# Optimization experiments

Hardware: AMD Instinct MI355X
Metric: run time of the kernel (lower is better)

Reference implementation:

```python
import jax, jax.numpy as jnp
import numpy as np

N_NODES = 50000


def setup_inputs() -> dict:
    key = jax.random.key(0)
    k1, k2, k3, k4 = jax.random.split(key, 4)
    x = jax.random.normal(k1, (N_NODES, 256), dtype=jnp.float32)
    edge_index = jax.random.randint(k2, (2, 800000), 0, N_NODES, dtype=jnp.int64)
    W1 = jax.random.normal(k3, (256, 128), dtype=jnp.float32) * (1.0 / np.sqrt(256))
    b1 = jnp.zeros((128,), dtype=jnp.float32)
    W2 = jax.random.normal(k4, (128, 16), dtype=jnp.float32) * (1.0 / np.sqrt(128))
    b2 = jnp.zeros((16,), dtype=jnp.float32)
    return {"x": x, "edge_index": edge_index, "W1": W1, "b1": b1, "W2": W2, "b2": b2}


def _gcn_norm(edge_index, num_nodes):
    # add self-loops, then symmetric normalization D^-1/2 A D^-1/2 (PyG GCNConv default)
    loop = jnp.arange(num_nodes, dtype=edge_index.dtype)
    src = jnp.concatenate([edge_index[0], loop])
    dst = jnp.concatenate([edge_index[1], loop])
    deg = jax.ops.segment_sum(jnp.ones_like(dst, dtype=jnp.float32), dst, num_segments=num_nodes)
    dinv = jnp.where(deg > 0, jax.lax.rsqrt(deg), 0.0)
    norm = dinv[src] * dinv[dst]  # [E+N]
    return src, dst, norm


def _gcn_conv(h, W, b, src, dst, norm, num_nodes):
    h = h @ W                             # linear before propagate
    msg = h[src] * norm[:, None]          # gather + edge scaling
    agg = jax.ops.segment_sum(msg, dst, num_segments=num_nodes)  # scatter-add
    return agg + b


def reference(x, edge_index, W1, b1, W2, b2):
    n = x.shape[0]
    src, dst, norm = _gcn_norm(edge_index, n)
    h = jax.nn.relu(_gcn_conv(x, W1, b1, src, dst, norm, n))
    # F.dropout(training=False) is identity in eval mode
    out = _gcn_conv(h, W2, b2, src, dst, norm, n)
    return jax.nn.log_softmax(out, axis=1)
```

## Files before the change

kernel.cpp:

```cpp
#include <hip/hip_runtime.h>
#include <hip/hip_bf16.h>
#include <math.h>


#define FIN 256
#define FH  128
#define FO  16
#define ECH_LOG 13
#define ECH (1 << ECH_LOG)
#define NCHUNK 98
#define WPH 6272

typedef unsigned int uint;
typedef unsigned short ushort;
typedef __attribute__((ext_vector_type(8))) short bf16x8;
typedef __attribute__((ext_vector_type(4))) float f32x4;

static __device__ __forceinline__ ushort f2bf(float f) {
    __hip_bfloat16 b = __float2bfloat16(f);
    return *reinterpret_cast<ushort*>(&b);
}
static __device__ __forceinline__ float bf2f(ushort u) {
    return __uint_as_float(((uint)u) << 16);
}

__global__ __launch_bounds__(256) void GCN_wprep_k(const float* __restrict__ W1,
                                                   ushort* __restrict__ whT,
                                                   ushort* __restrict__ wlT) {
    int i = blockIdx.x * 256 + threadIdx.x;
    int k = i >> 7, c = i & 127;
    float w = W1[i];
    ushort hh = f2bf(w);
    ushort hl = f2bf(w - bf2f(hh));
    whT[c * 256 + k] = hh;
    wlT[c * 256 + k] = hl;
}

#define G1_BR 64
#define G1_KC 32

__global__ __launch_bounds__(256, 4) void GCN_histgemm_k(
        const float* __restrict__ x, const ushort* __restrict__ whT,
        const ushort* __restrict__ wlT, ushort* __restrict__ h1,
        const int* __restrict__ edge, uint* __restrict__ cw,
        int* __restrict__ rank,
        int N, int E, int nHist, int nWords, int wph) {
    __shared__ __align__(16) char smem[WPH * 4];
    int tid = threadIdx.x;

    if ((int)blockIdx.x < nHist) {
        int bid = blockIdx.x;
        int half = bid & 1;
        int c = bid >> 1;
        uint* lh = (uint*)smem;
        int w0 = half * wph;
        int wlim = nWords - w0; if (wlim > wph) wlim = wph;
        for (int j = tid; j < wlim; j += 256) lh[j] = 0;
        __syncthreads();
        int base = c << ECH_LOG;
        int lim = base + ECH; if (lim > E) lim = E;
        for (int i = base + tid; i < lim; i += 256) {
            int d = edge[E + i];
            int wd = (d >> 2) - w0;
            if ((unsigned)wd < (unsigned)wlim) {
                int sh = (d & 3) << 3;
                uint old = atomicAdd(&lh[wd], 1u << sh);
                rank[i] = (int)((old >> sh) & 0xFFu);
            }
        }
        __syncthreads();
        for (int j = tid; j < wlim; j += 256)
            cw[(size_t)c * nWords + w0 + j] = lh[j];
        return;
    }

    ushort* xh_s = (ushort*)smem;
    ushort* xl_s = (ushort*)(smem + 4096);
    ushort* wh_s = (ushort*)(smem + 8192);
    ushort* wl_s = (ushort*)(smem + 16384);
    int row0 = (blockIdx.x - nHist) * G1_BR;
    int ln = tid & 63;
    int w  = tid >> 6;
    int ln15 = ln & 15;
    int q16  = ln >> 4;

    f32x4 acc[4][2];
    #pragma unroll
    for (int mr = 0; mr < 4; mr++)
        #pragma unroll
        for (int nc = 0; nc < 2; nc++) acc[mr][nc] = (f32x4){0.f, 0.f, 0.f, 0.f};

    for (int kc = 0; kc < FIN; kc += G1_KC) {
        #pragma unroll
        for (int j = 0; j < 2; j++) {
            int u = tid + j * 256;
            int r = u >> 3, kq = u & 7;
            int gr = row0 + r;
            float4 v = make_float4(0.f, 0.f, 0.f, 0.f);
            if (gr < N) v = *(const float4*)&x[(size_t)gr * FIN + kc + kq * 4];
            ushort h0 = f2bf(v.x), h1v = f2bf(v.y), h2 = f2bf(v.z), h3 = f2bf(v.w);
            ushort l0 = f2bf(v.x - bf2f(h0));
            ushort l1 = f2bf(v.y - bf2f(h1v));
            ushort l2 = f2bf(v.z - bf2f(h2));
            ushort l3 = f2bf(v.w - bf2f(h3));
            uint2 hw, lw;
            hw.x = (uint)h0 | ((uint)h1v << 16);
            hw.y = (uint)h2 | ((uint)h3 << 16);
            lw.x = (uint)l0 | ((uint)l1 << 16);
            lw.y = (uint)l2 | ((uint)l3 << 16);
            int byte = (r * 64 + kq * 8) ^ (((r >> 1) & 3) << 4);
            *(uint2*)((char*)xh_s + byte) = hw;
            *(uint2*)((char*)xl_s + byte) = lw;
        }
        #pragma unroll
        for (int j = 0; j < 2; j++) {
            int u = tid + j * 256;
            int c = u >> 2, ku = u & 3;
            uint4 vh = *(const uint4*)&whT[(size_t)c * 256 + kc + ku * 8];
            uint4 vl = *(const uint4*)&wlT[(size_t)c * 256 + kc + ku * 8];
            int byte = (c * 64 + ku * 16) ^ (((c >> 1) & 3) << 4);
            *(uint4*)((char*)wh_s + byte) = vh;
            *(uint4*)((char*)wl_s + byte) = vl;
        }
        __syncthreads();

        bf16x8 ah[4], al[4], bh[2], bl[2];
        #pragma unroll
        for (int mr = 0; mr < 4; mr++) {
            int r = mr * 16 + ln15;
            int byte = r * 64 + ((q16 * 16) ^ (((r >> 1) & 3) << 4));
            ah[mr] = *(const bf16x8*)((const char*)xh_s + byte);
            al[mr] = *(const bf16x8*)((const char*)xl_s + byte);
        }
        #pragma unroll
        for (int nc = 0; nc < 2; nc++) {
            int c = w * 32 + nc * 16 + ln15;
            int byte = c * 64 + ((q16 * 16) ^ (((c >> 1) & 3) << 4));
            bh[nc] = *(const bf16x8*)((const char*)wh_s + byte);
            bl[nc] = *(const bf16x8*)((const char*)wl_s + byte);
        }
        #pragma unroll
        for (int mr = 0; mr < 4; mr++)
            #pragma unroll
            for (int nc = 0; nc < 2; nc++) {
                acc[mr][nc] = __builtin_amdgcn_mfma_f32_16x16x32_bf16(
                    ah[mr], bh[nc], acc[mr][nc], 0, 0, 0);
                acc[mr][nc] = __builtin_amdgcn_mfma_f32_16x16x32_bf16(
                    al[mr], bh[nc], acc[mr][nc], 0, 0, 0);
                acc[mr][nc] = __builtin_amdgcn_mfma_f32_16x16x32_bf16(
                    ah[mr], bl[nc], acc[mr][nc], 0, 0, 0);
            }
        __syncthreads();
    }

    #pragma unroll
    for (int mr = 0; mr < 4; mr++) {
        #pragma unroll
        for (int nc = 0; nc < 2; nc++) {
            int cw2 = w * 32 + nc * 16 + ln15;
            #pragma unroll
            for (int j = 0; j < 4; j++) {
                int gr = row0 + mr * 16 + q16 * 4 + j;
                if (gr < N) h1[(size_t)gr * FH + cw2] = f2bf(acc[mr][nc][j]);
            }
        }
    }
}

__global__ __launch_bounds__(256) void GCN_chpfx_k(uint* __restrict__ cw,
                                                   int* __restrict__ count,
                                                   int* __restrict__ bsum,
                                                   int N, int nWords) {
    int tid = threadIdx.x;
    int w = blockIdx.x * 256 + tid;
    int local = 0;
    if (w < nWords) {
        uint s0 = 0, s1 = 0, s2 = 0, s3 = 0;
        for (int c = 0; c < NCHUNK; c++) {
            uint* p = &cw[(size_t)c * nWords + w];
            uint v = *p;
            *p = s0 | (s1 << 8) | (s2 << 16) | (s3 << 24);
            s0 += v & 0xFFu;
            s1 += (v >> 8) & 0xFFu;
            s2 += (v >> 16) & 0xFFu;
            s3 += (v >> 24) & 0xFFu;
        }
        int d0 = 4 * w;
        count[d0 + 0] = (int)s0;
        count[d0 + 1] = (int)s1;
        count[d0 + 2] = (int)s2;
        count[d0 + 3] = (int)s3;
        local = (int)(s0 + s1 + s2 + s3) + 4;
    }
    __shared__ int red[256];
    red[tid] = local;
    __syncthreads();
    for (int st = 32; st > 0; st >>= 1) {
        if ((tid & 63) < st) red[tid] += red[tid + st];
        __syncthreads();
    }
    if ((tid & 63) == 0) bsum[blockIdx.x * 4 + (tid >> 6)] = red[tid];
}

__global__ __launch_bounds__(256) void GCN_scan2_k(const int* __restrict__ count,
                                                   const int* __restrict__ bsum,
                                                   int2* __restrict__ rd2,
                                                   int2* __restrict__ edata, int N) {
    int tid = threadIdx.x;
    int b = blockIdx.x;
    int d = b * 256 + tid;
    int cnt1 = (d < N) ? count[d] + 1 : 0;

    __shared__ int red[256];
    int offp = 0;
    for (int t = tid; t < b; t += 256) offp += bsum[t];
    red[tid] = offp;
    __syncthreads();
    for (int st = 128; st > 0; st >>= 1) {
        if (tid < st) red[tid] += red[tid + st];
        __syncthreads();
    }
    int blockOff = red[0];
    __syncthreads();

    __shared__ int ssum[256];
    ssum[tid] = cnt1;
    __syncthreads();
    for (int off = 1; off < 256; off <<= 1) {
        int t = (tid >= off) ? ssum[tid - off] : 0;
        __syncthreads();
        ssum[tid] += t;
        __syncthreads();
    }
    int r = blockOff + ssum[tid] - cnt1;

    if (d < N) {
        float dv = rsqrtf((float)cnt1);
        rd2[d] = make_int2(r, __float_as_int(dv));
        edata[r] = make_int2(d, __float_as_int(dv * dv));
    }
    if (b == gridDim.x - 1 && tid == 255) rd2[N] = make_int2(blockOff + ssum[255], 0);
}

__global__ __launch_bounds__(256) void GCN_fill_k(const int* __restrict__ edge,
                                                  const int* __restrict__ rank,
                                                  const uint* __restrict__ cw,
                                                  const int2* __restrict__ rd2,
                                                  int2* __restrict__ edata,
                                                  int E, int nWords) {
    int i = blockIdx.x * 256 + threadIdx.x;
    if (i >= E) return;
    int s = edge[i];
    int d = edge[E + i];
    int rk = rank[i];
    int c = i >> ECH_LOG;
    uint pw = cw[(size_t)c * nWords + (d >> 2)];
    int pfx = (int)((pw >> ((d & 3) << 3)) & 0xFFu);
    int2 rdd = rd2[d];
    float ds = __int_as_float(rd2[s].y);
    edata[rdd.x + 1 + pfx + rk] =
        make_int2(s, __float_as_int(ds * __int_as_float(rdd.y)));
}

__global__ __launch_bounds__(256) void GCN_agg1gemm2_k(
        const ushort* __restrict__ h1, const int2* __restrict__ rd2,
        const int2* __restrict__ ed, const float* __restrict__ b1,
        const float* __restrict__ W2, ushort* __restrict__ h2b, int N) {
    __shared__ float w2s[FH][FO];
    __shared__ float hs[16][FH + 4];
    int tid = threadIdx.x;
    #pragma unroll
    for (int j = 0; j < (FH * FO) / 256; j++) {
        int i = tid + j * 256;
        w2s[i >> 4][i & 15] = W2[i];
    }

    int node0 = blockIdx.x * 16;
    int local = tid >> 4;
    int j = tid & 15;
    int node = node0 + local;

    if (node < N) {
        int beg = rd2[node].x, end = rd2[node + 1].x;
        const uint4* hp = (const uint4*)h1;

        float a[8];
        #pragma unroll
        for (int t = 0; t < 8; t++) a[t] = 0.f;

        int i = beg;
        for (; i + 4 <= end; i += 4) {
            int2 e0 = ed[i + 0], e1 = ed[i + 1], e2 = ed[i + 2], e3 = ed[i + 3];
            float w0 = __int_as_float(e0.y), w1 = __int_as_float(e1.y);
            float w2 = __int_as_float(e2.y), w3 = __int_as_float(e3.y);
            uint4 g0 = hp[(size_t)e0.x * 16 + j];
            uint4 g1 = hp[(size_t)e1.x * 16 + j];
            uint4 g2 = hp[(size_t)e2.x * 16 + j];
            uint4 g3 = hp[(size_t)e3.x * 16 + j];
            #pragma unroll
            for (int q = 0; q < 4; q++) {
                uint u0 = (&g0.x)[q], u1 = (&g1.x)[q], u2 = (&g2.x)[q], u3 = (&g3.x)[q];
                a[q*2+0] += __uint_as_float(u0 << 16) * w0;
                a[q*2+1] += __uint_as_float(u0 & 0xFFFF0000u) * w0;
                a[q*2+0] += __uint_as_float(u1 << 16) * w1;
                a[q*2+1] += __uint_as_float(u1 & 0xFFFF0000u) * w1;
                a[q*2+0] += __uint_as_float(u2 << 16) * w2;
                a[q*2+1] += __uint_as_float(u2 & 0xFFFF0000u) * w2;
                a[q*2+0] += __uint_as_float(u3 << 16) * w3;
                a[q*2+1] += __uint_as_float(u3 & 0xFFFF0000u) * w3;
            }
        }
        for (; i < end; i++) {
            int2 e = ed[i];
            float w = __int_as_float(e.y);
            uint4 g = hp[(size_t)e.x * 16 + j];
            #pragma unroll
            for (int q = 0; q < 4; q++) {
                uint u = (&g.x)[q];
                a[q*2+0] += __uint_as_float(u << 16) * w;
                a[q*2+1] += __uint_as_float(u & 0xFFFF0000u) * w;
            }
        }

        const float4* bp = (const float4*)b1;
        float4 bb0 = bp[j * 2 + 0];
        float4 bb1 = bp[j * 2 + 1];
        float4 o0, o1;
        o0.x = fmaxf(a[0] + bb0.x, 0.f);
        o0.y = fmaxf(a[1] + bb0.y, 0.f);
        o0.z = fmaxf(a[2] + bb0.z, 0.f);
        o0.w = fmaxf(a[3] + bb0.w, 0.f);
        o1.x = fmaxf(a[4] + bb1.x, 0.f);
        o1.y = fmaxf(a[5] + bb1.y, 0.f);
        o1.z = fmaxf(a[6] + bb1.z, 0.f);
        o1.w = fmaxf(a[7] + bb1.w, 0.f);
        *(float4*)&hs[local][j * 8 + 0] = o0;
        *(float4*)&hs[local][j * 8 + 4] = o1;
    }
    __syncthreads();

    float acc = 0.f;
    #pragma unroll 8
    for (int k = 0; k < FH; k++) acc += hs[local][k] * w2s[k][j];
    if (node < N) h2b[(size_t)node * FO + j] = f2bf(acc);
}

__global__ __launch_bounds__(256) void GCN_agg2_k(const ushort* __restrict__ h2b,
                                                  const int2* __restrict__ rd2,
                                                  const int2* __restrict__ ed,
                                                  const float* __restrict__ b2,
                                                  float* __restrict__ out, int N) {
    int tid = threadIdx.x;
    int node = blockIdx.x * 32 + (tid >> 3);
    if (node >= N) return;
    int f2 = tid & 7;
    int beg = rd2[node].x, end = rd2[node + 1].x;
    const uint* hp = (const uint*)h2b;
    float a0 = 0.f, a1 = 0.f;
    int i = beg;
    for (; i + 4 <= end; i += 4) {
        int2 e0 = ed[i + 0], e1 = ed[i + 1], e2 = ed[i + 2], e3 = ed[i + 3];
        uint u0 = hp[(size_t)e0.x * 8 + f2];
        uint u1 = hp[(size_t)e1.x * 8 + f2];
        uint u2 = hp[(size_t)e2.x * 8 + f2];
        uint u3 = hp[(size_t)e3.x * 8 + f2];
        float w0 = __int_as_float(e0.y), w1 = __int_as_float(e1.y);
        float w2 = __int_as_float(e2.y), w3 = __int_as_float(e3.y);
        a0 += __uint_as_float(u0 << 16) * w0 + __uint_as_float(u1 << 16) * w1
            + __uint_as_float(u2 << 16) * w2 + __uint_as_float(u3 << 16) * w3;
        a1 += __uint_as_float(u0 & 0xFFFF0000u) * w0 + __uint_as_float(u1 & 0xFFFF0000u) * w1
            + __uint_as_float(u2 & 0xFFFF0000u) * w2 + __uint_as_float(u3 & 0xFFFF0000u) * w3;
    }
    for (; i < end; i++) {
        int2 e = ed[i];
        uint u = hp[(size_t)e.x * 8 + f2];
        float w = __int_as_float(e.y);
        a0 += __uint_as_float(u << 16) * w;
        a1 += __uint_as_float(u & 0xFFFF0000u) * w;
    }
    float2 bb = ((const float2*)b2)[f2];
    float v0 = a0 + bb.x;
    float v1 = a1 + bb.y;
    float mx = fmaxf(v0, v1);
    #pragma unroll
    for (int m = 4; m >= 1; m >>= 1) mx = fmaxf(mx, __shfl_xor(mx, m, 8));
    float s = expf(v0 - mx) + expf(v1 - mx);
    #pragma unroll
    for (int m = 4; m >= 1; m >>= 1) s += __shfl_xor(s, m, 8);
    float ls = logf(s);
    float2 o = make_float2(v0 - mx - ls, v1 - mx - ls);
    ((float2*)out)[(size_t)node * 8 + f2] = o;
}

extern "C" void kernel_launch(void* const* d_in, const int* in_sizes, int n_in,
                              void* d_out, int out_size, void* d_ws, size_t ws_size,
                              hipStream_t stream) {
    (void)n_in; (void)out_size; (void)ws_size;
    const float* x  = (const float*)d_in[0];
    const int*   edp = (const int*)d_in[1];
    const float* W1 = (const float*)d_in[2];
    const float* b1 = (const float*)d_in[3];
    const float* W2 = (const float*)d_in[4];
    const float* b2 = (const float*)d_in[5];
    float* out = (float*)d_out;

    int N = in_sizes[0] / FIN;
    int E = in_sizes[1] / 2;
    int M = E + N;
    int nWords = (N + 3) / 4;
    int wph = (nWords + 1) / 2;
    int nScanBlocks = (N + 255) / 256;
    int nChpfx = (nWords + 255) / 256;

    char* p = (char*)d_ws;
    auto take = [&](size_t bytes) -> char* {
        char* r = p;
        p += (bytes + 255) & ~(size_t)255;
        return r;
    };
    int*    count  = (int*)take((size_t)N * 4);
    int*    rank   = (int*)take((size_t)E * 4);
    uint*   cw     = (uint*)take((size_t)NCHUNK * nWords * 4);
    int2*   rd2    = (int2*)take((size_t)(N + 1) * 8);
    int*    bsum   = (int*)take((size_t)(4 * nChpfx) * 4);
    int2*   edata  = (int2*)take((size_t)M * 8);
    ushort* whT    = (ushort*)take((size_t)FH * FIN * 2);
    ushort* wlT    = (ushort*)take((size_t)FH * FIN * 2);
    ushort* h1     = (ushort*)take((size_t)N * FH * 2);
    ushort* h2b    = (ushort*)take((size_t)N * FO * 2);

    int eBlocks = (E + 255) / 256;
    int nGemm   = (N + G1_BR - 1) / G1_BR;
    int nHist   = 2 * NCHUNK;

    GCN_wprep_k<<<(FIN * FH) / 256, 256, 0, stream>>>(W1, whT, wlT);
    GCN_histgemm_k<<<nHist + nGemm, 256, 0, stream>>>(
        x, whT, wlT, h1, edp, cw, rank, N, E, nHist, nWords, wph);
    GCN_chpfx_k<<<nChpfx, 256, 0, stream>>>(cw, count, bsum, N, nWords);
    GCN_scan2_k<<<nScanBlocks, 256, 0, stream>>>(count, bsum, rd2, edata, N);
    GCN_fill_k<<<eBlocks, 256, 0, stream>>>(edp, rank, cw, rd2, edata, E, nWords);
    GCN_agg1gemm2_k<<<(N + 15) / 16, 256, 0, stream>>>(h1, rd2, edata, b1, W2, h2b, N);
    GCN_agg2_k<<<(N + 31) / 32, 256, 0, stream>>>(h2b, rd2, edata, b2, out, N);
}
```

Measured before the change: 116.3 us.

## Drop x low-part MFMA, split chunk prefix across waves, unroll gathers by 8

The first GEMM no longer splits x into high and low bf16 parts. This removes one of three MFMAs and the matching LDS stores and loads, at some cost in precision. The chunk prefix kernel now spreads the 98 chunks over four wave groups and combines their partial sums through shared memory, raising parallelism on that serial loop. The two aggregation kernels get an 8-way unrolled gather loop so more independent loads are in flight per thread.

```diff
diff --git a/kernel.cpp b/kernel.cpp
--- a/kernel.cpp
+++ b/kernel.cpp
@@ -75,9 +75,8 @@
     }
 
     ushort* xh_s = (ushort*)smem;
-    ushort* xl_s = (ushort*)(smem + 4096);
-    ushort* wh_s = (ushort*)(smem + 8192);
-    ushort* wl_s = (ushort*)(smem + 16384);
+    ushort* wh_s = (ushort*)(smem + 4096);
+    ushort* wl_s = (ushort*)(smem + 12288);
     int row0 = (blockIdx.x - nHist) * G1_BR;
     int ln = tid & 63;
     int w  = tid >> 6;
@@ -98,19 +97,11 @@
             int gr = row0 + r;
             float4 v = make_float4(0.f, 0.f, 0.f, 0.f);
             if (gr < N) v = *(const float4*)&x[(size_t)gr * FIN + kc + kq * 4];
-            ushort h0 = f2bf(v.x), h1v = f2bf(v.y), h2 = f2bf(v.z), h3 = f2bf(v.w);
-            ushort l0 = f2bf(v.x - bf2f(h0));
-            ushort l1 = f2bf(v.y - bf2f(h1v));
-            ushort l2 = f2bf(v.z - bf2f(h2));
-            ushort l3 = f2bf(v.w - bf2f(h3));
-            uint2 hw, lw;
-            hw.x = (uint)h0 | ((uint)h1v << 16);
-            hw.y = (uint)h2 | ((uint)h3 << 16);
-            lw.x = (uint)l0 | ((uint)l1 << 16);
-            lw.y = (uint)l2 | ((uint)l3 << 16);
+            uint2 hw;
+            hw.x = (uint)f2bf(v.x) | ((uint)f2bf(v.y) << 16);
+            hw.y = (uint)f2bf(v.z) | ((uint)f2bf(v.w) << 16);
             int byte = (r * 64 + kq * 8) ^ (((r >> 1) & 3) << 4);
             *(uint2*)((char*)xh_s + byte) = hw;
-            *(uint2*)((char*)xl_s + byte) = lw;
         }
         #pragma unroll
         for (int j = 0; j < 2; j++) {
@@ -124,13 +115,12 @@
         }
         __syncthreads();
 
-        bf16x8 ah[4], al[4], bh[2], bl[2];
+        bf16x8 ah[4], bh[2], bl[2];
         #pragma unroll
         for (int mr = 0; mr < 4; mr++) {
             int r = mr * 16 + ln15;
             int byte = r * 64 + ((q16 * 16) ^ (((r >> 1) & 3) << 4));
             ah[mr] = *(const bf16x8*)((const char*)xh_s + byte);
-            al[mr] = *(const bf16x8*)((const char*)xl_s + byte);
         }
         #pragma unroll
         for (int nc = 0; nc < 2; nc++) {
@@ -146,8 +136,6 @@
                 acc[mr][nc] = __builtin_amdgcn_mfma_f32_16x16x32_bf16(
                     ah[mr], bh[nc], acc[mr][nc], 0, 0, 0);
                 acc[mr][nc] = __builtin_amdgcn_mfma_f32_16x16x32_bf16(
-                    al[mr], bh[nc], acc[mr][nc], 0, 0, 0);
-                acc[mr][nc] = __builtin_amdgcn_mfma_f32_16x16x32_bf16(
                     ah[mr], bl[nc], acc[mr][nc], 0, 0, 0);
             }
         __syncthreads();
@@ -171,35 +159,66 @@
                                                    int* __restrict__ count,
                                                    int* __restrict__ bsum,
                                                    int N, int nWords) {
+    __shared__ int part[4][64][4];
+    __shared__ int red[64];
     int tid = threadIdx.x;
-    int w = blockIdx.x * 256 + tid;
-    int local = 0;
+    int wl = tid & 63, g = tid >> 6;
+    int w = blockIdx.x * 64 + wl;
+    int c0 = g * 25;
+    int c1 = c0 + 25; if (c1 > NCHUNK) c1 = NCHUNK;
+
+    int s0 = 0, s1 = 0, s2 = 0, s3 = 0;
     if (w < nWords) {
-        uint s0 = 0, s1 = 0, s2 = 0, s3 = 0;
-        for (int c = 0; c < NCHUNK; c++) {
+        for (int c = c0; c < c1; c++) {
+            uint v = cw[(size_t)c * nWords + w];
+            s0 += (int)(v & 0xFFu);
+            s1 += (int)((v >> 8) & 0xFFu);
+            s2 += (int)((v >> 16) & 0xFFu);
+            s3 += (int)((v >> 24) & 0xFFu);
+        }
+    }
+    part[g][wl][0] = s0; part[g][wl][1] = s1;
+    part[g][wl][2] = s2; part[g][wl][3] = s3;
+    __syncthreads();
+
+    int b0 = 0, b1 = 0, b2 = 0, b3 = 0;
+    for (int gg = 0; gg < g; gg++) {
+        b0 += part[gg][wl][0]; b1 += part[gg][wl][1];
+        b2 += part[gg][wl][2]; b3 += part[gg][wl][3];
+    }
+    if (w < nWords) {
+        uint r0 = (uint)b0, r1 = (uint)b1, r2 = (uint)b2, r3 = (uint)b3;
+        for (int c = c0; c < c1; c++) {
             uint* p = &cw[(size_t)c * nWords + w];
             uint v = *p;
-            *p = s0 | (s1 << 8) | (s2 << 16) | (s3 << 24);
-            s0 += v & 0xFFu;
-            s1 += (v >> 8) & 0xFFu;
-            s2 += (v >> 16) & 0xFFu;
-            s3 += (v >> 24) & 0xFFu;
-        }
+            *p = (r0 & 0xFFu) | ((r1 & 0xFFu) << 8) | ((r2 & 0xFFu) << 16) | ((r3 & 0xFFu) << 24);
+            r0 += v & 0xFFu;
+            r1 += (v >> 8) & 0xFFu;
+            r2 += (v >> 16) & 0xFFu;
+            r3 += (v >> 24) & 0xFFu;
+        }
+    }
+    int local = 0;
+    if (g == 3 && w < nWords) {
+        int t0 = b0 + s0, t1 = b1 + s1, t2 = b2 + s2, t3 = b3 + s3;
         int d0 = 4 * w;
-        count[d0 + 0] = (int)s0;
-        count[d0 + 1] = (int)s1;
-        count[d0 + 2] = (int)s2;
-        count[d0 + 3] = (int)s3;
-        local = (int)(s0 + s1 + s2 + s3) + 4;
-    }
-    __shared__ int red[256];
-    red[tid] = local;
-    __syncthreads();
-    for (int st = 32; st > 0; st >>= 1) {
-        if ((tid & 63) < st) red[tid] += red[tid + st];
-        __syncthreads();
-    }
-    if ((tid & 63) == 0) bsum[blockIdx.x * 4 + (tid >> 6)] = red[tid];
+        if (d0 + 0 < N) count[d0 + 0] = t0;
+        if (d0 + 1 < N) count[d0 + 1] = t1;
+        if (d0 + 2 < N) count[d0 + 2] = t2;
+        if (d0 + 3 < N) count[d0 + 3] = t3;
+        local = t0 + t1 + t2 + t3 + 4;
+    }
+    if (g == 3) red[wl] = local;
+    __syncthreads();
+    if (tid < 32) { red[tid] += red[tid + 32]; }
+    __syncthreads();
+    if (tid < 16) { red[tid] += red[tid + 16]; }
+    __syncthreads();
+    if (tid < 8) { red[tid] += red[tid + 8]; }
+    __syncthreads();
+    if (tid < 4) { red[tid] += red[tid + 4]; }
+    __syncthreads();
+    if (tid == 0) bsum[blockIdx.x] = red[0] + red[1] + red[2] + red[3];
 }
 
 __global__ __launch_bounds__(256) void GCN_scan2_k(const int* __restrict__ count,
@@ -289,6 +308,24 @@
         for (int t = 0; t < 8; t++) a[t] = 0.f;
 
         int i = beg;
+        for (; i + 8 <= end; i += 8) {
+            int2 e[8];
+            uint4 gg[8];
+            #pragma unroll
+            for (int t = 0; t < 8; t++) e[t] = ed[i + t];
+            #pragma unroll
+            for (int t = 0; t < 8; t++) gg[t] = hp[(size_t)e[t].x * 16 + j];
+            #pragma unroll
+            for (int t = 0; t < 8; t++) {
+                float w = __int_as_float(e[t].y);
+                #pragma unroll
+                for (int q = 0; q < 4; q++) {
+                    uint u = (&gg[t].x)[q];
+                    a[q*2+0] += __uint_as_float(u << 16) * w;
+                    a[q*2+1] += __uint_as_float(u & 0xFFFF0000u) * w;
+                }
+            }
+        }
         for (; i + 4 <= end; i += 4) {
             int2 e0 = ed[i + 0], e1 = ed[i + 1], e2 = ed[i + 2], e3 = ed[i + 3];
             float w0 = __int_as_float(e0.y), w1 = __int_as_float(e1.y);
@@ -358,6 +395,20 @@
     const uint* hp = (const uint*)h2b;
     float a0 = 0.f, a1 = 0.f;
     int i = beg;
+    for (; i + 8 <= end; i += 8) {
+        int2 e[8];
+        uint u[8];
+        #pragma unroll
+        for (int t = 0; t < 8; t++) e[t] = ed[i + t];
+        #pragma unroll
+        for (int t = 0; t < 8; t++) u[t] = hp[(size_t)e[t].x * 8 + f2];
+        #pragma unroll
+        for (int t = 0; t < 8; t++) {
+            float w = __int_as_float(e[t].y);
+            a0 += __uint_as_float(u[t] << 16) * w;
+            a1 += __uint_as_float(u[t] & 0xFFFF0000u) * w;
+        }
+    }
     for (; i + 4 <= end; i += 4) {
         int2 e0 = ed[i + 0], e1 = ed[i + 1], e2 = ed[i + 2], e3 = ed[i + 3];
         uint u0 = hp[(size_t)e0.x * 8 + f2];
@@ -410,7 +461,7 @@
     int nWords = (N + 3) / 4;
     int wph = (nWords + 1) / 2;
     int nScanBlocks = (N + 255) / 256;
-    int nChpfx = (nWords + 255) / 256;
+    int nChpfx = (nWords + 63) / 64;
 
     char* p = (char*)d_ws;
     auto take = [&](size_t bytes) -> char* {
@@ -422,7 +473,7 @@
     int*    rank   = (int*)take((size_t)E * 4);
     uint*   cw     = (uint*)take((size_t)NCHUNK * nWords * 4);
     int2*   rd2    = (int2*)take((size_t)(N + 1) * 8);
-    int*    bsum   = (int*)take((size_t)(4 * nChpfx) * 4);
+    int*    bsum   = (int*)take((size_t)nChpfx * 4);
     int2*   edata  = (int2*)take((size_t)M * 8);
     ushort* whT    = (ushort*)take((size_t)FH * FIN * 2);
     ushort* wlT    = (ushort*)take((size_t)FH * FIN * 2);
```

Measured after the change: 113.4 us. 2.5% less time.
